# Optimization experiments

Hardware: AMD Instinct MI355X
Metric: run time of the kernel (lower is better)

Reference implementation:

```python
import jax, jax.numpy as jnp
from jax import lax
import numpy as np

N = 65536
D = 512
NUM_STEPS = 10
TIME_INTERVAL = 1.0


def setup_inputs() -> dict:
    key = jax.random.key(0)
    ks = jax.random.split(key, 8)
    s1 = 1.0 / np.sqrt(D + 1)
    s2 = 1.0 / np.sqrt(D)
    sg = 1.0 / np.sqrt(2 * D)
    return {
        "current_node_features": jax.random.normal(ks[0], (N, D), jnp.float32),
        "previous_hidden_state": jax.random.normal(ks[1], (N, D), jnp.float32),
        # torch nn.Linear layout: weight [out, in], bias [out]
        "W1": jax.random.uniform(ks[2], (D, D + 1), jnp.float32, -s1, s1),
        "b1": jax.random.uniform(ks[3], (D,), jnp.float32, -s1, s1),
        "W2": jax.random.uniform(ks[4], (D, D), jnp.float32, -s2, s2),
        "b2": jax.random.uniform(ks[5], (D,), jnp.float32, -s2, s2),
        "Wg": jax.random.uniform(ks[6], (D, 2 * D), jnp.float32, -sg, sg),
        "bg": jax.random.uniform(ks[7], (D,), jnp.float32, -sg, sg),
    }


def reference(current_node_features, previous_hidden_state, W1, b1, W2, b2, Wg, bg):
    x = current_node_features
    dt = jnp.asarray(TIME_INTERVAL / NUM_STEPS, x.dtype)
    n = x.shape[0]

    def euler_step(h, t):
        # concat time feature: [N, D+1]
        time_col = jnp.full((n, 1), t, h.dtype)
        z = jnp.concatenate([h, time_col], axis=-1)
        deriv = jnp.tanh(jnp.tanh(z @ W1.T + b1) @ W2.T + b2)
        return h + dt * deriv, None

    ts = jnp.arange(NUM_STEPS, dtype=x.dtype) * dt  # t_i = start + i*dt
    evolved, _ = lax.scan(euler_step, previous_hidden_state, ts)

    combined = jnp.concatenate([x, evolved], axis=-1)  # [N, 2D]
    gate = jax.nn.sigmoid(combined @ Wg.T + bg)
    updated = gate * evolved + (1.0 - gate) * x
    return updated, updated
```

## Files before the change

kernel.cpp:

```cpp
#include <hip/hip_runtime.h>

#define N_ROWS 65536
#define DIM    512
#define NSTEP  10

typedef float  f32x16 __attribute__((ext_vector_type(16)));
typedef float  f32x4  __attribute__((ext_vector_type(4)));
typedef short  s16x8  __attribute__((ext_vector_type(8)));
typedef __bf16 bf16x8 __attribute__((ext_vector_type(8)));
typedef unsigned int u32x2 __attribute__((ext_vector_type(2)));
typedef unsigned int u32x4 __attribute__((ext_vector_type(4)));

__device__ __forceinline__ unsigned f2bf(float f) {
  unsigned u = __float_as_uint(f);
  return (u + 0x7fffu + ((u >> 16) & 1u)) >> 16;
}
__device__ __forceinline__ unsigned pack2bf_rn(float a, float b) {
  unsigned ua = __float_as_uint(a) + 0x8000u;
  unsigned ub = __float_as_uint(b) + 0x8000u;
  return __builtin_amdgcn_perm(ub, ua, 0x07060302u);
}
#define LOG2E_X2 2.885390081777927f
#define LOG2E    1.442695040888963f
__device__ __forceinline__ float ftanh(float x) {
  float t = __builtin_amdgcn_exp2f(x * LOG2E_X2);
  float r = __builtin_amdgcn_rcpf(1.0f + t);
  return __builtin_fmaf(-2.0f, r, 1.0f);
}
__device__ __forceinline__ float fsigm(float x) {
  float t = __builtin_amdgcn_exp2f(-x * LOG2E);
  return __builtin_amdgcn_rcpf(1.0f + t);
}
__device__ __forceinline__ void mfma(f32x16& c, s16x8 a, s16x8 b) {
  c = __builtin_amdgcn_mfma_f32_32x32x16_bf16(
        __builtin_bit_cast(bf16x8, a), __builtin_bit_cast(bf16x8, b), c, 0, 0, 0);
}

__global__ void pack_frags_kernel(const float* __restrict__ src, int row_stride,
                                  int col_off, unsigned short* __restrict__ dst) {
  const int idx = blockIdx.x * 256 + threadIdx.x;
  const int l    = idx & 63;
  const int frag = idx >> 6;
  const int otg  = frag >> 5;
  const int ks   = frag & 31;
  const int o = otg * 32 + (l & 31);
  const int k = ks * 16 + (l >> 5) * 8;
  const float* p = src + (size_t)o * row_stride + col_off + k;
  s16x8 v;
#pragma unroll
  for (int i = 0; i < 8; ++i) v[i] = (short)f2bf(p[i]);
  *reinterpret_cast<s16x8*>(dst + (size_t)idx * 8) = v;
}

__global__ void c1_kernel(const float* __restrict__ W1, const float* __restrict__ b1,
                          float* __restrict__ c1) {
  const int o = threadIdx.x;
  const float wt = W1[(size_t)o * 513 + 512];
  const float bb = b1[o];
  for (int s = 0; s < NSTEP; ++s)
    c1[s * DIM + o] = bb + ((float)s * 0.1f) * wt;
}

__global__ __launch_bounds__(1024)
void ode_fused(const float* __restrict__ x, const float* __restrict__ h0,
               const float* __restrict__ b2, const float* __restrict__ bg,
               const s16x8* __restrict__ w1f, const s16x8* __restrict__ w2f,
               const s16x8* __restrict__ wgaf, const s16x8* __restrict__ wgbf,
               const float* __restrict__ c1, float* __restrict__ out)
{
  __shared__ char ldsT[64 * 1024];

  const int tid = threadIdx.x;
  const int w   = tid >> 6;
  const int l   = tid & 63;
  const int lm  = l & 31;
  const int h5  = l >> 5;
  const int m0  = blockIdx.x << 6;
  const int ow  = w << 5;
  const unsigned lbyte = (unsigned)l << 4;

  {
#pragma unroll
    for (int q = 0; q < 2; ++q) {
      const int ks = (w << 1) | q;
#pragma unroll
      for (int mt = 0; mt < 2; ++mt) {
        const float* src = h0 + (size_t)(m0 + (mt << 5) + lm) * DIM + (ks << 4) + (h5 << 3);
        f32x4 v0 = *reinterpret_cast<const f32x4*>(src);
        f32x4 v1 = *reinterpret_cast<const f32x4*>(src + 4);
        u32x4 pk;
        pk[0] = pack2bf_rn(v0[0], v0[1]); pk[1] = pack2bf_rn(v0[2], v0[3]);
        pk[2] = pack2bf_rn(v1[0], v1[1]); pk[3] = pack2bf_rn(v1[2], v1[3]);
        *reinterpret_cast<u32x4*>(ldsT + (((ks << 1) | mt) << 10) + lbyte) = pk;
      }
    }
  }

  f32x16 hst[2];
#pragma unroll
  for (int mt = 0; mt < 2; ++mt) {
    const float* hr = h0 + (size_t)(m0 + (mt << 5) + lm) * DIM;
#pragma unroll
    for (int g = 0; g < 4; ++g) {
      const int oc = ow + (g << 3) + (h5 << 2);
      f32x4 v = *reinterpret_cast<const f32x4*>(hr + oc);
#pragma unroll
      for (int j = 0; j < 4; ++j) hst[mt][(g << 2) + j] = v[j];
    }
  }

  f32x16 acc[2];

  auto mm_lds = [&](const s16x8* __restrict__ A) {
    const s16x8* Aw = A + (w << 11);
#pragma unroll 4
    for (int ks = 0; ks < 32; ++ks) {
      s16x8 a  = Aw[(ks << 6) + l];
      s16x8 b0 = *reinterpret_cast<const s16x8*>(ldsT + (ks << 11) + lbyte);
      s16x8 b1 = *reinterpret_cast<const s16x8*>(ldsT + (ks << 11) + 1024 + lbyte);
      mfma(acc[0], a, b0);
      mfma(acc[1], a, b1);
    }
  };

  auto acc_init = [&](const float* __restrict__ vec) {
#pragma unroll
    for (int g = 0; g < 4; ++g) {
      const int oc = ow + (g << 3) + (h5 << 2);
      f32x4 v = *reinterpret_cast<const f32x4*>(vec + oc);
#pragma unroll
      for (int j = 0; j < 4; ++j) {
        acc[0][(g << 2) + j] = v[j];
        acc[1][(g << 2) + j] = v[j];
      }
    }
  };

  auto tile_write = [&](const f32x16 src[2]) {
    const unsigned base = ((unsigned)w << 12) + ((unsigned)lm << 4) + ((unsigned)h5 << 3);
#pragma unroll
    for (int mt = 0; mt < 2; ++mt)
#pragma unroll
      for (int g = 0; g < 4; ++g) {
        u32x2 pk;
        pk[0] = pack2bf_rn(src[mt][(g << 2) + 0], src[mt][(g << 2) + 1]);
        pk[1] = pack2bf_rn(src[mt][(g << 2) + 2], src[mt][(g << 2) + 3]);
        *reinterpret_cast<u32x2*>(ldsT + base + ((g >> 1) << 11) + (mt << 10) + ((g & 1) << 9)) = pk;
      }
  };

  __syncthreads();

#pragma unroll 1
  for (int s = 0; s < NSTEP; ++s) {
    acc_init(c1 + s * DIM);
    mm_lds(w1f);
#pragma unroll
    for (int mt = 0; mt < 2; ++mt)
#pragma unroll
      for (int i = 0; i < 16; ++i) acc[mt][i] = ftanh(acc[mt][i]);
    __syncthreads();
    tile_write(acc);
    __syncthreads();
    acc_init(b2);
    mm_lds(w2f);
#pragma unroll
    for (int mt = 0; mt < 2; ++mt)
#pragma unroll
      for (int i = 0; i < 16; ++i) {
        float t = __builtin_amdgcn_exp2f(acc[mt][i] * LOG2E_X2);
        float r = __builtin_amdgcn_rcpf(1.0f + t);
        hst[mt][i] = __builtin_fmaf(-0.2f, r, hst[mt][i] + 0.1f);
      }
    __syncthreads();
    tile_write(hst);
    __syncthreads();
  }

  acc_init(bg);
  mm_lds(wgbf);
  {
    const s16x8* Aw = wgaf + (w << 11);
    const float* xr0 = x + (size_t)(m0 + lm) * DIM + (h5 << 3);
    const float* xr1 = xr0 + (size_t)32 * DIM;
#pragma unroll 4
    for (int ks = 0; ks < 32; ++ks) {
      s16x8 a = Aw[(ks << 6) + l];
      const int kc = ks << 4;
      f32x4 u0 = *reinterpret_cast<const f32x4*>(xr0 + kc);
      f32x4 u1 = *reinterpret_cast<const f32x4*>(xr0 + kc + 4);
      u32x4 pb;
      pb[0] = pack2bf_rn(u0[0], u0[1]); pb[1] = pack2bf_rn(u0[2], u0[3]);
      pb[2] = pack2bf_rn(u1[0], u1[1]); pb[3] = pack2bf_rn(u1[2], u1[3]);
      s16x8 b0 = __builtin_bit_cast(s16x8, pb);
      f32x4 w0 = *reinterpret_cast<const f32x4*>(xr1 + kc);
      f32x4 w1 = *reinterpret_cast<const f32x4*>(xr1 + kc + 4);
      u32x4 qb;
      qb[0] = pack2bf_rn(w0[0], w0[1]); qb[1] = pack2bf_rn(w0[2], w0[3]);
      qb[2] = pack2bf_rn(w1[0], w1[1]); qb[3] = pack2bf_rn(w1[2], w1[3]);
      s16x8 b1 = __builtin_bit_cast(s16x8, qb);
      mfma(acc[0], a, b0);
      mfma(acc[1], a, b1);
    }
  }

  float* out1 = out + (size_t)N_ROWS * DIM;
#pragma unroll
  for (int mt = 0; mt < 2; ++mt) {
    const int m = m0 + (mt << 5) + lm;
    const float* xr = x + (size_t)m * DIM;
    float* o0p = out  + (size_t)m * DIM;
    float* o1p = out1 + (size_t)m * DIM;
#pragma unroll
    for (int g = 0; g < 4; ++g) {
      const int oc = ow + (g << 3) + (h5 << 2);
      f32x4 xv = *reinterpret_cast<const f32x4*>(xr + oc);
      f32x4 r;
#pragma unroll
      for (int j = 0; j < 4; ++j) {
        const float gt = fsigm(acc[mt][(g << 2) + j]);
        const float ev = hst[mt][(g << 2) + j];
        r[j] = gt * ev + (1.0f - gt) * xv[j];
      }
      *reinterpret_cast<f32x4*>(o0p + oc) = r;
      *reinterpret_cast<f32x4*>(o1p + oc) = r;
    }
  }
}

extern "C" void kernel_launch(void* const* d_in, const int* in_sizes, int n_in,
                              void* d_out, int out_size, void* d_ws, size_t ws_size,
                              hipStream_t stream) {
  const float* x  = (const float*)d_in[0];
  const float* h0 = (const float*)d_in[1];
  const float* W1 = (const float*)d_in[2];
  const float* b1 = (const float*)d_in[3];
  const float* W2 = (const float*)d_in[4];
  const float* b2 = (const float*)d_in[5];
  const float* Wg = (const float*)d_in[6];
  const float* bg = (const float*)d_in[7];

  char* ws = (char*)d_ws;
  const size_t FRAG_BYTES = (size_t)512 * 512 * 2;
  unsigned short* w1f  = (unsigned short*)(ws + 0 * FRAG_BYTES);
  unsigned short* w2f  = (unsigned short*)(ws + 1 * FRAG_BYTES);
  unsigned short* wgaf = (unsigned short*)(ws + 2 * FRAG_BYTES);
  unsigned short* wgbf = (unsigned short*)(ws + 3 * FRAG_BYTES);
  float*          c1   = (float*)(ws + 4 * FRAG_BYTES);

  pack_frags_kernel<<<128, 256, 0, stream>>>(W1, 513, 0,   w1f);
  pack_frags_kernel<<<128, 256, 0, stream>>>(W2, 512, 0,   w2f);
  pack_frags_kernel<<<128, 256, 0, stream>>>(Wg, 1024, 0,  wgaf);
  pack_frags_kernel<<<128, 256, 0, stream>>>(Wg, 1024, 512, wgbf);
  c1_kernel<<<1, 512, 0, stream>>>(W1, b1, c1);

  ode_fused<<<N_ROWS / 64, 1024, 0, stream>>>(x, h0, b2, bg,
                                              (const s16x8*)w1f, (const s16x8*)w2f,
                                              (const s16x8*)wgaf, (const s16x8*)wgbf,
                                              c1, (float*)d_out);
}
```

Measured before the change: 1.084 ms.

## Halve block to 8 waves, give each wave 64 output columns, prefetch weight fragments

The block shrinks from 16 to 8 waves, and each wave now computes two 32-column output tiles. Every LDS B fragment read therefore feeds four MFMAs instead of two. The weight-fragment loads in mm_lds are software-pipelined with a 4-deep register prefetch ring. Launch bounds change to 512 threads with 2 blocks per CU, which aims for more blocks per CU and better LDS reuse. The cost is double the accumulator and hidden-state registers per thread, which risks spills or lower occupancy.

```diff
diff --git a/kernel.cpp b/kernel.cpp
--- a/kernel.cpp
+++ b/kernel.cpp
@@ -61,7 +61,7 @@
     c1[s * DIM + o] = bb + ((float)s * 0.1f) * wt;
 }
 
-__global__ __launch_bounds__(1024)
+__global__ __launch_bounds__(512, 2)
 void ode_fused(const float* __restrict__ x, const float* __restrict__ h0,
                const float* __restrict__ b2, const float* __restrict__ bg,
                const s16x8* __restrict__ w1f, const s16x8* __restrict__ w2f,
@@ -76,77 +76,100 @@
   const int lm  = l & 31;
   const int h5  = l >> 5;
   const int m0  = blockIdx.x << 6;
-  const int ow  = w << 5;
+  const int ow  = w << 6;
   const unsigned lbyte = (unsigned)l << 4;
 
   {
 #pragma unroll
-    for (int q = 0; q < 2; ++q) {
-      const int ks = (w << 1) | q;
-#pragma unroll
-      for (int mt = 0; mt < 2; ++mt) {
-        const float* src = h0 + (size_t)(m0 + (mt << 5) + lm) * DIM + (ks << 4) + (h5 << 3);
-        f32x4 v0 = *reinterpret_cast<const f32x4*>(src);
-        f32x4 v1 = *reinterpret_cast<const f32x4*>(src + 4);
-        u32x4 pk;
-        pk[0] = pack2bf_rn(v0[0], v0[1]); pk[1] = pack2bf_rn(v0[2], v0[3]);
-        pk[2] = pack2bf_rn(v1[0], v1[1]); pk[3] = pack2bf_rn(v1[2], v1[3]);
-        *reinterpret_cast<u32x4*>(ldsT + (((ks << 1) | mt) << 10) + lbyte) = pk;
+    for (int q = 0; q < 8; ++q) {
+      const int f  = (w << 3) | q;
+      const int ks = f >> 1;
+      const int mt = f & 1;
+      const float* src = h0 + (size_t)(m0 + (mt << 5) + lm) * DIM + (ks << 4) + (h5 << 3);
+      f32x4 v0 = *reinterpret_cast<const f32x4*>(src);
+      f32x4 v1 = *reinterpret_cast<const f32x4*>(src + 4);
+      u32x4 pk;
+      pk[0] = pack2bf_rn(v0[0], v0[1]); pk[1] = pack2bf_rn(v0[2], v0[3]);
+      pk[2] = pack2bf_rn(v1[0], v1[1]); pk[3] = pack2bf_rn(v1[2], v1[3]);
+      *reinterpret_cast<u32x4*>(ldsT + (f << 10) + lbyte) = pk;
+    }
+  }
+
+  f32x16 hst[2][2];
+#pragma unroll
+  for (int ot = 0; ot < 2; ++ot)
+#pragma unroll
+    for (int mt = 0; mt < 2; ++mt) {
+      const float* hr = h0 + (size_t)(m0 + (mt << 5) + lm) * DIM;
+#pragma unroll
+      for (int g = 0; g < 4; ++g) {
+        const int oc = ow + (ot << 5) + (g << 3) + (h5 << 2);
+        f32x4 v = *reinterpret_cast<const f32x4*>(hr + oc);
+#pragma unroll
+        for (int j = 0; j < 4; ++j) hst[ot][mt][(g << 2) + j] = v[j];
       }
     }
-  }
-
-  f32x16 hst[2];
-#pragma unroll
-  for (int mt = 0; mt < 2; ++mt) {
-    const float* hr = h0 + (size_t)(m0 + (mt << 5) + lm) * DIM;
-#pragma unroll
-    for (int g = 0; g < 4; ++g) {
-      const int oc = ow + (g << 3) + (h5 << 2);
-      f32x4 v = *reinterpret_cast<const f32x4*>(hr + oc);
-#pragma unroll
-      for (int j = 0; j < 4; ++j) hst[mt][(g << 2) + j] = v[j];
-    }
-  }
-
-  f32x16 acc[2];
+
+  f32x16 acc[2][2];
 
   auto mm_lds = [&](const s16x8* __restrict__ A) {
-    const s16x8* Aw = A + (w << 11);
+    const s16x8* A0 = A + (w << 12);
+    const s16x8* A1 = A0 + 2048;
+    s16x8 a0[4], a1[4];
+#pragma unroll
+    for (int i = 0; i < 4; ++i) { a0[i] = A0[(i << 6) + l]; a1[i] = A1[(i << 6) + l]; }
 #pragma unroll 4
-    for (int ks = 0; ks < 32; ++ks) {
-      s16x8 a  = Aw[(ks << 6) + l];
+    for (int ks = 0; ks < 28; ++ks) {
+      s16x8 ca0 = a0[ks & 3], ca1 = a1[ks & 3];
+      a0[ks & 3] = A0[((ks + 4) << 6) + l];
+      a1[ks & 3] = A1[((ks + 4) << 6) + l];
       s16x8 b0 = *reinterpret_cast<const s16x8*>(ldsT + (ks << 11) + lbyte);
       s16x8 b1 = *reinterpret_cast<const s16x8*>(ldsT + (ks << 11) + 1024 + lbyte);
-      mfma(acc[0], a, b0);
-      mfma(acc[1], a, b1);
+      mfma(acc[0][0], ca0, b0);
+      mfma(acc[0][1], ca0, b1);
+      mfma(acc[1][0], ca1, b0);
+      mfma(acc[1][1], ca1, b1);
+    }
+#pragma unroll
+    for (int ks = 28; ks < 32; ++ks) {
+      s16x8 ca0 = a0[ks & 3], ca1 = a1[ks & 3];
+      s16x8 b0 = *reinterpret_cast<const s16x8*>(ldsT + (ks << 11) + lbyte);
+      s16x8 b1 = *reinterpret_cast<const s16x8*>(ldsT + (ks << 11) + 1024 + lbyte);
+      mfma(acc[0][0], ca0, b0);
+      mfma(acc[0][1], ca0, b1);
+      mfma(acc[1][0], ca1, b0);
+      mfma(acc[1][1], ca1, b1);
     }
   };
 
   auto acc_init = [&](const float* __restrict__ vec) {
 #pragma unroll
-    for (int g = 0; g < 4; ++g) {
-      const int oc = ow + (g << 3) + (h5 << 2);
-      f32x4 v = *reinterpret_cast<const f32x4*>(vec + oc);
-#pragma unroll
-      for (int j = 0; j < 4; ++j) {
-        acc[0][(g << 2) + j] = v[j];
-        acc[1][(g << 2) + j] = v[j];
+    for (int ot = 0; ot < 2; ++ot)
+#pragma unroll
+      for (int g = 0; g < 4; ++g) {
+        const int oc = ow + (ot << 5) + (g << 3) + (h5 << 2);
+        f32x4 v = *reinterpret_cast<const f32x4*>(vec + oc);
+#pragma unroll
+        for (int mt = 0; mt < 2; ++mt)
+#pragma unroll
+          for (int j = 0; j < 4; ++j) acc[ot][mt][(g << 2) + j] = v[j];
       }
-    }
   };
 
-  auto tile_write = [&](const f32x16 src[2]) {
-    const unsigned base = ((unsigned)w << 12) + ((unsigned)lm << 4) + ((unsigned)h5 << 3);
-#pragma unroll
-    for (int mt = 0; mt < 2; ++mt)
-#pragma unroll
-      for (int g = 0; g < 4; ++g) {
-        u32x2 pk;
-        pk[0] = pack2bf_rn(src[mt][(g << 2) + 0], src[mt][(g << 2) + 1]);
-        pk[1] = pack2bf_rn(src[mt][(g << 2) + 2], src[mt][(g << 2) + 3]);
-        *reinterpret_cast<u32x2*>(ldsT + base + ((g >> 1) << 11) + (mt << 10) + ((g & 1) << 9)) = pk;
-      }
+  auto tile_write = [&](const f32x16 src[2][2]) {
+    const unsigned base = ((unsigned)w << 13) + ((unsigned)lm << 4) + ((unsigned)h5 << 3);
+#pragma unroll
+    for (int ot = 0; ot < 2; ++ot)
+#pragma unroll
+      for (int mt = 0; mt < 2; ++mt)
+#pragma unroll
+        for (int g = 0; g < 4; ++g) {
+          u32x2 pk;
+          pk[0] = pack2bf_rn(src[ot][mt][(g << 2) + 0], src[ot][mt][(g << 2) + 1]);
+          pk[1] = pack2bf_rn(src[ot][mt][(g << 2) + 2], src[ot][mt][(g << 2) + 3]);
+          *reinterpret_cast<u32x2*>(ldsT + base + (ot << 12) + ((g >> 1) << 11)
+                                    + (mt << 10) + ((g & 1) << 9)) = pk;
+        }
   };
 
   __syncthreads();
@@ -156,22 +179,26 @@
     acc_init(c1 + s * DIM);
     mm_lds(w1f);
 #pragma unroll
-    for (int mt = 0; mt < 2; ++mt)
-#pragma unroll
-      for (int i = 0; i < 16; ++i) acc[mt][i] = ftanh(acc[mt][i]);
+    for (int ot = 0; ot < 2; ++ot)
+#pragma unroll
+      for (int mt = 0; mt < 2; ++mt)
+#pragma unroll
+        for (int i = 0; i < 16; ++i) acc[ot][mt][i] = ftanh(acc[ot][mt][i]);
     __syncthreads();
     tile_write(acc);
     __syncthreads();
     acc_init(b2);
     mm_lds(w2f);
 #pragma unroll
-    for (int mt = 0; mt < 2; ++mt)
-#pragma unroll
-      for (int i = 0; i < 16; ++i) {
-        float t = __builtin_amdgcn_exp2f(acc[mt][i] * LOG2E_X2);
-        float r = __builtin_amdgcn_rcpf(1.0f + t);
-        hst[mt][i] = __builtin_fmaf(-0.2f, r, hst[mt][i] + 0.1f);
-      }
+    for (int ot = 0; ot < 2; ++ot)
+#pragma unroll
+      for (int mt = 0; mt < 2; ++mt)
+#pragma unroll
+        for (int i = 0; i < 16; ++i) {
+          float t = __builtin_amdgcn_exp2f(acc[ot][mt][i] * LOG2E_X2);
+          float r = __builtin_amdgcn_rcpf(1.0f + t);
+          hst[ot][mt][i] = __builtin_fmaf(-0.2f, r, hst[ot][mt][i] + 0.1f);
+        }
     __syncthreads();
     tile_write(hst);
     __syncthreads();
@@ -180,12 +207,14 @@
   acc_init(bg);
   mm_lds(wgbf);
   {
-    const s16x8* Aw = wgaf + (w << 11);
+    const s16x8* A0 = wgaf + (w << 12);
+    const s16x8* A1 = A0 + 2048;
     const float* xr0 = x + (size_t)(m0 + lm) * DIM + (h5 << 3);
     const float* xr1 = xr0 + (size_t)32 * DIM;
 #pragma unroll 4
     for (int ks = 0; ks < 32; ++ks) {
-      s16x8 a = Aw[(ks << 6) + l];
+      s16x8 a0 = A0[(ks << 6) + l];
+      s16x8 a1 = A1[(ks << 6) + l];
       const int kc = ks << 4;
       f32x4 u0 = *reinterpret_cast<const f32x4*>(xr0 + kc);
       f32x4 u1 = *reinterpret_cast<const f32x4*>(xr0 + kc + 4);
@@ -199,8 +228,10 @@
       qb[0] = pack2bf_rn(w0[0], w0[1]); qb[1] = pack2bf_rn(w0[2], w0[3]);
       qb[2] = pack2bf_rn(w1[0], w1[1]); qb[3] = pack2bf_rn(w1[2], w1[3]);
       s16x8 b1 = __builtin_bit_cast(s16x8, qb);
-      mfma(acc[0], a, b0);
-      mfma(acc[1], a, b1);
+      mfma(acc[0][0], a0, b0);
+      mfma(acc[0][1], a0, b1);
+      mfma(acc[1][0], a1, b0);
+      mfma(acc[1][1], a1, b1);
     }
   }
 
@@ -212,19 +243,21 @@
     float* o0p = out  + (size_t)m * DIM;
     float* o1p = out1 + (size_t)m * DIM;
 #pragma unroll
-    for (int g = 0; g < 4; ++g) {
-      const int oc = ow + (g << 3) + (h5 << 2);
-      f32x4 xv = *reinterpret_cast<const f32x4*>(xr + oc);
-      f32x4 r;
-#pragma unroll
-      for (int j = 0; j < 4; ++j) {
-        const float gt = fsigm(acc[mt][(g << 2) + j]);
-        const float ev = hst[mt][(g << 2) + j];
-        r[j] = gt * ev + (1.0f - gt) * xv[j];
+    for (int ot = 0; ot < 2; ++ot)
+#pragma unroll
+      for (int g = 0; g < 4; ++g) {
+        const int oc = ow + (ot << 5) + (g << 3) + (h5 << 2);
+        f32x4 xv = *reinterpret_cast<const f32x4*>(xr + oc);
+        f32x4 r;
+#pragma unroll
+        for (int j = 0; j < 4; ++j) {
+          const float gt = fsigm(acc[ot][mt][(g << 2) + j]);
+          const float ev = hst[ot][mt][(g << 2) + j];
+          r[j] = gt * ev + (1.0f - gt) * xv[j];
+        }
+        *reinterpret_cast<f32x4*>(o0p + oc) = r;
+        *reinterpret_cast<f32x4*>(o1p + oc) = r;
       }
-      *reinterpret_cast<f32x4*>(o0p + oc) = r;
-      *reinterpret_cast<f32x4*>(o1p + oc) = r;
-    }
   }
 }
 
@@ -254,8 +287,8 @@
   pack_frags_kernel<<<128, 256, 0, stream>>>(Wg, 1024, 512, wgbf);
   c1_kernel<<<1, 512, 0, stream>>>(W1, b1, c1);
 
-  ode_fused<<<N_ROWS / 64, 1024, 0, stream>>>(x, h0, b2, bg,
-                                              (const s16x8*)w1f, (const s16x8*)w2f,
-                                              (const s16x8*)wgaf, (const s16x8*)wgbf,
-                                              c1, (float*)d_out);
-}
+  ode_fused<<<N_ROWS / 64, 512, 0, stream>>>(x, h0, b2, bg,
+                                             (const s16x8*)w1f, (const s16x8*)w2f,
+                                             (const s16x8*)wgaf, (const s16x8*)wgbf,
+                                             c1, (float*)d_out);
+}
```

New measurement: 1.054 ms. 2.8% less time.
